# Kernel tuning notes

Measured on AMD Instinct MI355X. Metric: run time of the kernel, lower is better.

The kernel has to match this reference:

```python
import jax, jax.numpy as jnp
import numpy as np

EID, EMB, HID, IN_DIM = 30000, 256, 512, 3
SRC_T, TRG_T, B = 128, 50, 64


def _gru_step(x, h, W_ih, W_hh, b_ih, b_hh):
    # torch GRU gate math. W_ih: [3H, in], W_hh: [3H, H]
    gi = x @ W_ih.T + b_ih
    gh = h @ W_hh.T + b_hh
    i_r, i_z, i_n = jnp.split(gi, 3, axis=1)
    h_r, h_z, h_n = jnp.split(gh, 3, axis=1)
    r = jax.nn.sigmoid(i_r + h_r)
    z = jax.nn.sigmoid(i_z + h_z)
    n = jnp.tanh(i_n + r * h_n)
    return (1.0 - z) * n + z * h


def setup_inputs() -> dict:
    key = jax.random.key(0)
    ks = jax.random.split(key, 24)
    s = 0.05
    inp = {
        "src": jax.random.normal(ks[0], (SRC_T, B, IN_DIM), jnp.float32),
        "src_len": jax.random.randint(ks[1], (B,), SRC_T // 2, SRC_T + 1).astype(jnp.int32),
        "trg_eid": jax.random.randint(ks[2], (TRG_T, B), 0, EID),
        "trg_rate": jax.random.uniform(ks[3], (TRG_T, B), jnp.float32),
        # encoder GRU
        "W_ih_enc": jax.random.normal(ks[4], (3 * HID, IN_DIM), jnp.float32) * s,
        "W_hh_enc": jax.random.normal(ks[5], (3 * HID, HID), jnp.float32) * s,
        "b_ih_enc": jnp.zeros((3 * HID,), jnp.float32),
        "b_hh_enc": jnp.zeros((3 * HID,), jnp.float32),
        # decoder embedding + GRUCell (input = emb + rate_size(1))
        "emb_dec": jax.random.normal(ks[6], (EID, EMB), jnp.float32) * s,
        "W_ih_dec": jax.random.normal(ks[7], (3 * HID, EMB + 1), jnp.float32) * s,
        "W_hh_dec": jax.random.normal(ks[8], (3 * HID, HID), jnp.float32) * s,
        "b_ih_dec": jnp.zeros((3 * HID,), jnp.float32),
        "b_hh_dec": jnp.zeros((3 * HID,), jnp.float32),
        # multi-task block (has its own embedding table)
        "emb_mt": jax.random.normal(ks[9], (EID, EMB), jnp.float32) * s,
        "W_eid": jax.random.normal(ks[10], (EID, HID), jnp.float32) * s,
        "b_eid": jnp.zeros((EID,), jnp.float32),
        "W_r1": jax.random.normal(ks[11], (HID, HID + EMB), jnp.float32) * s,
        "b_r1": jnp.zeros((HID,), jnp.float32),
        "W_r2": jax.random.normal(ks[12], (1, HID), jnp.float32) * s,
        "b_r2": jnp.zeros((1,), jnp.float32),
    }
    return inp


def reference(src, src_len, trg_eid, trg_rate,
              W_ih_enc, W_hh_enc, b_ih_enc, b_hh_enc,
              emb_dec, W_ih_dec, W_hh_dec, b_ih_dec, b_hh_dec,
              emb_mt, W_eid, b_eid, W_r1, b_r1, W_r2, b_r2):
    Bsz = src.shape[1]
    h0 = jnp.zeros((Bsz, HID), src.dtype)

    # --- Encoder: packed GRU == masked scan; final hidden frozen at each seq's length ---
    def enc_step(h, xt_t):
        x_t, t = xt_t
        h_new = _gru_step(x_t, h, W_ih_enc, W_hh_enc, b_ih_enc, b_hh_enc)
        h = jnp.where((t < src_len)[:, None], h_new, h)
        return h, None

    ts = jnp.arange(src.shape[0])
    hidden, _ = jax.lax.scan(enc_step, h0, (src, ts))  # [B, H]

    def dec_step(carry, _):
        h, eid, rate = carry
        x = jnp.concatenate([emb_dec[eid], rate[:, None]], axis=1)  # [B, EMB+1]
        h = _gru_step(x, h, W_ih_dec, W_hh_dec, b_ih_dec, b_hh_dec)
        pre_eid = jax.nn.log_softmax(h @ W_eid.T + b_eid, axis=1)   # [B, EID]
        idx = jnp.argmax(pre_eid, axis=1)
        r1 = jnp.concatenate([emb_mt[idx], h], axis=1) @ W_r1.T + b_r1
        pre_rate = jax.nn.sigmoid((jax.nn.relu(r1) @ W_r2.T + b_r2)[:, 0])  # [B]
        return (h, idx, pre_rate), (pre_eid, pre_rate)

    init = (hidden, trg_eid[0], trg_rate[0])
    _, (eids, rates) = jax.lax.scan(dec_step, init, None, length=TRG_T - 1)

    eid_result = jnp.concatenate([jnp.zeros((1, Bsz, EID), src.dtype), eids], axis=0)
    rate_result = jnp.concatenate([jnp.zeros((1, Bsz), src.dtype), rates], axis=0)
    return eid_result, rate_result
```

## Files before the change

### kernel.cpp

```cpp
#include <hip/hip_runtime.h>
#include <cmath>

#define EIDN  30000
#define EMBN  256
#define HIDN  512
#define INDIM 3
#define SRCT  128
#define TRGT  50
#define BN    64
#define G3H   1536
#define WIH_PAD 260

struct alignas(16) WS {
  float wihd[G3H * WIH_PAD];
  float hb[2][BN][HIDN];
  float rowsum[BN];
  float rate_cur[BN];
  int   eid_cur[BN];
  unsigned long long amax[BN];
};

__device__ __forceinline__ float sigmoidf_(float x) { return 1.f / (1.f + expf(-x)); }

__device__ __forceinline__ unsigned int orderf_(float f) {
  unsigned int b = __float_as_uint(f);
  return b ^ ((b & 0x80000000u) ? 0xFFFFFFFFu : 0x80000000u);
}

__device__ __forceinline__ unsigned long long shfl_down_u64(unsigned long long v, int off, int w) {
  unsigned int lo = (unsigned int)v;
  unsigned int hi = (unsigned int)(v >> 32);
  lo = __shfl_down(lo, off, w);
  hi = __shfl_down(hi, off, w);
  return ((unsigned long long)hi << 32) | (unsigned long long)lo;
}

__device__ __forceinline__ void dot6(const float* __restrict__ x,
                                     const float* const* __restrict__ w,
                                     int n4, float* __restrict__ acc) {
  const float4* x4 = (const float4*)x;
#pragma unroll 4
  for (int k = 0; k < n4; ++k) {
    float4 xv = x4[k];
#pragma unroll
    for (int i = 0; i < 6; ++i) {
      float4 wv = ((const float4*)w[i])[k];
      acc[i] = fmaf(xv.w, wv.w, fmaf(xv.z, wv.z, fmaf(xv.y, wv.y, fmaf(xv.x, wv.x, acc[i]))));
    }
  }
}

__global__ void k_init(const float* __restrict__ Wih_d,
                       const int* __restrict__ trg_eid,
                       const float* __restrict__ trg_rate,
                       float* __restrict__ out, WS* __restrict__ ws) {
  int gid = blockIdx.x * blockDim.x + threadIdx.x;
  int nt = gridDim.x * blockDim.x;
  const int N = G3H * 257;
  for (int i = gid; i < N; i += nt) {
    int r = i / 257, c = i - r * 257;
    ws->wihd[r * WIH_PAD + c] = Wih_d[i];
  }
  float* hb0 = &ws->hb[0][0][0];
  for (int i = gid; i < BN * HIDN; i += nt) hb0[i] = 0.f;
  if (gid < BN) {
    ws->eid_cur[gid]  = trg_eid[gid];
    ws->rate_cur[gid] = trg_rate[gid];
    out[(size_t)TRGT * BN * EIDN + gid] = 0.f;
  }
}

__global__ __launch_bounds__(256) void k_enc_step(
    const float* __restrict__ src, const int* __restrict__ src_len,
    const float* __restrict__ Wih, const float* __restrict__ bih,
    const float* __restrict__ bhh, const float* __restrict__ Whh,
    const float* __restrict__ hin, float* __restrict__ hout, int t) {
  __shared__ float part[BN][4][6];
  int tid = threadIdx.x;
  int b = tid & 63, kq = tid >> 6;
  int j0 = blockIdx.x * 2;

  const float* wrows[6];
#pragma unroll
  for (int idx = 0; idx < 6; ++idx) {
    int u = idx / 3, g = idx - 3 * u;
    wrows[idx] = Whh + (size_t)(g * HIDN + j0 + u) * HIDN + kq * 128;
  }
  float acc[6] = {0.f, 0.f, 0.f, 0.f, 0.f, 0.f};
  dot6(hin + b * HIDN + kq * 128, wrows, 32, acc);
#pragma unroll
  for (int idx = 0; idx < 6; ++idx) part[b][kq][idx] = acc[idx];
  __syncthreads();

  if (kq == 0) {
    int len = src_len[b];
    const float* x = src + ((size_t)t * BN + b) * INDIM;
    float x0 = x[0], x1 = x[1], x2 = x[2];
#pragma unroll
    for (int u = 0; u < 2; ++u) {
      int j = j0 + u;
      float hg[3], ig[3];
#pragma unroll
      for (int g = 0; g < 3; ++g) {
        int idx = u * 3 + g;
        hg[g] = part[b][0][idx] + part[b][1][idx] + part[b][2][idx] + part[b][3][idx]
                + bhh[g * HIDN + j];
        int row = g * HIDN + j;
        ig[g] = bih[row] + x0 * Wih[row * 3] + x1 * Wih[row * 3 + 1] + x2 * Wih[row * 3 + 2];
      }
      float r = sigmoidf_(ig[0] + hg[0]);
      float z = sigmoidf_(ig[1] + hg[1]);
      float n = tanhf(ig[2] + r * hg[2]);
      float ho = hin[b * HIDN + j];
      hout[b * HIDN + j] = (t < len) ? ((1.f - z) * n + z * ho) : ho;
    }
  }
}

__global__ __launch_bounds__(256) void k_dec_gru(
    const float* __restrict__ emb_dec, const float* __restrict__ Whh,
    const float* __restrict__ bih, const float* __restrict__ bhh,
    WS* __restrict__ ws, const float* __restrict__ hin, float* __restrict__ hout) {
  __shared__ float partx[BN][4][6];
  __shared__ float parth[BN][4][6];
  int tid = threadIdx.x;
  if (blockIdx.x == 0 && tid < BN) {
    ws->rowsum[tid] = 0.f;
    ws->amax[tid] = 0ULL;
  }
  int b = tid & 63, kq = tid >> 6;
  int j0 = blockIdx.x * 2;
  int eid = ws->eid_cur[b];
  const float* xe = emb_dec + (size_t)eid * EMBN;
  const float* hrow = hin + b * HIDN;

  float accx[6] = {0.f, 0.f, 0.f, 0.f, 0.f, 0.f};
  float acch[6] = {0.f, 0.f, 0.f, 0.f, 0.f, 0.f};
  const float* w[6];

  if (kq == 0) {
#pragma unroll
    for (int idx = 0; idx < 6; ++idx) {
      int u = idx / 3, g = idx - 3 * u;
      w[idx] = ws->wihd + (size_t)(g * HIDN + j0 + u) * WIH_PAD;
    }
    dot6(xe, w, 48, accx);
  } else if (kq == 1) {
    float rate = ws->rate_cur[b];
#pragma unroll
    for (int idx = 0; idx < 6; ++idx) {
      int u = idx / 3, g = idx - 3 * u;
      const float* wr = ws->wihd + (size_t)(g * HIDN + j0 + u) * WIH_PAD;
      w[idx] = wr + 192;
      accx[idx] = rate * wr[256];
    }
    dot6(xe + 192, w, 16, accx);
#pragma unroll
    for (int idx = 0; idx < 6; ++idx) {
      int u = idx / 3, g = idx - 3 * u;
      w[idx] = Whh + (size_t)(g * HIDN + j0 + u) * HIDN;
    }
    dot6(hrow, w, 32, acch);
  } else {
    int off = (kq == 2) ? 128 : 320;
#pragma unroll
    for (int idx = 0; idx < 6; ++idx) {
      int u = idx / 3, g = idx - 3 * u;
      w[idx] = Whh + (size_t)(g * HIDN + j0 + u) * HIDN + off;
    }
    dot6(hrow + off, w, 48, acch);
  }
#pragma unroll
  for (int idx = 0; idx < 6; ++idx) {
    partx[b][kq][idx] = accx[idx];
    parth[b][kq][idx] = acch[idx];
  }
  __syncthreads();

  if (kq == 0) {
#pragma unroll
    for (int u = 0; u < 2; ++u) {
      int j = j0 + u;
      float ix[3], hh[3];
#pragma unroll
      for (int g = 0; g < 3; ++g) {
        int idx = u * 3 + g;
        ix[g] = partx[b][0][idx] + partx[b][1][idx] + partx[b][2][idx] + partx[b][3][idx]
                + bih[g * HIDN + j];
        hh[g] = parth[b][0][idx] + parth[b][1][idx] + parth[b][2][idx] + parth[b][3][idx]
                + bhh[g * HIDN + j];
      }
      float r = sigmoidf_(ix[0] + hh[0]);
      float z = sigmoidf_(ix[1] + hh[1]);
      float n = tanhf(ix[2] + r * hh[2]);
      hout[b * HIDN + j] = (1.f - z) * n + z * hin[b * HIDN + j];
    }
  }
}

__global__ __launch_bounds__(256) void k_logits(
    const float* __restrict__ Weid, const float* __restrict__ beid,
    const float* __restrict__ h, float* __restrict__ oslice,
    WS* __restrict__ ws) {
  __shared__ float sh[64][68];
  __shared__ float sw[64][68];
  int tid = threadIdx.x;
  int tr = tid >> 4, tc = tid & 15;
  int c0 = blockIdx.x * 64;
  float acc[4][4];
#pragma unroll
  for (int i = 0; i < 4; ++i)
#pragma unroll
    for (int m = 0; m < 4; ++m) acc[i][m] = 0.f;

  for (int kc = 0; kc < 8; ++kc) {
    int k0 = kc * 64;
#pragma unroll
    for (int u = 0; u < 4; ++u) {
      int flat = tid + u * 256;
      int r = flat >> 4, k4 = flat & 15;
      float4 hv = *(const float4*)(h + r * HIDN + k0 + k4 * 4);
      sh[k4 * 4 + 0][r] = hv.x; sh[k4 * 4 + 1][r] = hv.y;
      sh[k4 * 4 + 2][r] = hv.z; sh[k4 * 4 + 3][r] = hv.w;
      int c = c0 + r;
      float4 wv = make_float4(0.f, 0.f, 0.f, 0.f);
      if (c < EIDN) wv = *(const float4*)(Weid + (size_t)c * HIDN + k0 + k4 * 4);
      sw[k4 * 4 + 0][r] = wv.x; sw[k4 * 4 + 1][r] = wv.y;
      sw[k4 * 4 + 2][r] = wv.z; sw[k4 * 4 + 3][r] = wv.w;
    }
    __syncthreads();
#pragma unroll 8
    for (int kk = 0; kk < 64; ++kk) {
      float4 av = *(const float4*)&sh[kk][4 * tr];
      float4 bv = *(const float4*)&sw[kk][4 * tc];
      acc[0][0] = fmaf(av.x, bv.x, acc[0][0]); acc[0][1] = fmaf(av.x, bv.y, acc[0][1]);
      acc[0][2] = fmaf(av.x, bv.z, acc[0][2]); acc[0][3] = fmaf(av.x, bv.w, acc[0][3]);
      acc[1][0] = fmaf(av.y, bv.x, acc[1][0]); acc[1][1] = fmaf(av.y, bv.y, acc[1][1]);
      acc[1][2] = fmaf(av.y, bv.z, acc[1][2]); acc[1][3] = fmaf(av.y, bv.w, acc[1][3]);
      acc[2][0] = fmaf(av.z, bv.x, acc[2][0]); acc[2][1] = fmaf(av.z, bv.y, acc[2][1]);
      acc[2][2] = fmaf(av.z, bv.z, acc[2][2]); acc[2][3] = fmaf(av.z, bv.w, acc[2][3]);
      acc[3][0] = fmaf(av.w, bv.x, acc[3][0]); acc[3][1] = fmaf(av.w, bv.y, acc[3][1]);
      acc[3][2] = fmaf(av.w, bv.z, acc[3][2]); acc[3][3] = fmaf(av.w, bv.w, acc[3][3]);
    }
    __syncthreads();
  }

  int cbase = c0 + 4 * tc;
  float sume[4] = {0.f, 0.f, 0.f, 0.f};
  unsigned long long key[4] = {0ULL, 0ULL, 0ULL, 0ULL};
  if (cbase + 3 < EIDN) {
    float4 bb = *(const float4*)(beid + cbase);
#pragma unroll
    for (int i = 0; i < 4; ++i) {
      float4 L;
      L.x = acc[i][0] + bb.x; L.y = acc[i][1] + bb.y;
      L.z = acc[i][2] + bb.z; L.w = acc[i][3] + bb.w;
      *(float4*)(oslice + (size_t)(4 * tr + i) * EIDN + cbase) = L;
      sume[i] = expf(L.x) + expf(L.y) + expf(L.z) + expf(L.w);
      float lv[4] = {L.x, L.y, L.z, L.w};
#pragma unroll
      for (int cc = 0; cc < 4; ++cc) {
        unsigned long long pk = ((unsigned long long)orderf_(lv[cc]) << 32) |
                                (unsigned long long)(0xFFFFFFFFu - (unsigned)(cbase + cc));
        if (pk > key[i]) key[i] = pk;
      }
    }
  }
#pragma unroll
  for (int off = 8; off > 0; off >>= 1) {
#pragma unroll
    for (int i = 0; i < 4; ++i) {
      sume[i] += __shfl_down(sume[i], off, 16);
      unsigned long long o = shfl_down_u64(key[i], off, 16);
      if (o > key[i]) key[i] = o;
    }
  }
  if (tc == 0) {
#pragma unroll
    for (int i = 0; i < 4; ++i) {
      int r = 4 * tr + i;
      atomicAdd(&ws->rowsum[r], sume[i]);
      atomicMax(&ws->amax[r], key[i]);
    }
  }
}

__global__ __launch_bounds__(256) void k_finalize(
    float* __restrict__ oslice, float* __restrict__ rate_out,
    const float* __restrict__ emb_mt, const float* __restrict__ Wr1,
    const float* __restrict__ br1, const float* __restrict__ Wr2,
    const float* __restrict__ br2, const float* __restrict__ h,
    WS* __restrict__ ws) {
  int tid = threadIdx.x;
  __shared__ float logs[BN];
  if (tid < BN) logs[tid] = logf(ws->rowsum[tid]);
  __syncthreads();
  int gid = blockIdx.x * blockDim.x + tid;
  int nt = gridDim.x * blockDim.x;
  const int nf4 = BN * EIDN / 4;
  const int rowf4 = EIDN / 4;
  float4* o4 = (float4*)oslice;
  for (int f = gid; f < nf4; f += nt) {
    int b = f / rowf4;
    float lb = logs[b];
    float4 v = o4[f];
    v.x -= lb; v.y -= lb; v.z -= lb; v.w -= lb;
    o4[f] = v;
  }
  if (blockIdx.x < BN) {
    int b = blockIdx.x;
    int idx = (int)(0xFFFFFFFFu - (unsigned)(ws->amax[b] & 0xFFFFFFFFull));
    __shared__ float cat[EMBN + HIDN];
    cat[tid]       = emb_mt[(size_t)idx * EMBN + tid];
    cat[EMBN + tid]       = h[b * HIDN + tid];
    cat[EMBN + 256 + tid] = h[b * HIDN + 256 + tid];
    __syncthreads();
    const float4* c4 = (const float4*)cat;
    int j0 = tid * 2;
    const float4* w0 = (const float4*)(Wr1 + (size_t)j0 * (EMBN + HIDN));
    const float4* w1 = (const float4*)(Wr1 + (size_t)(j0 + 1) * (EMBN + HIDN));
    float a0 = br1[j0], a1 = br1[j0 + 1];
#pragma unroll 4
    for (int k = 0; k < (EMBN + HIDN) / 4; ++k) {
      float4 cv = c4[k];
      float4 v0 = w0[k], v1 = w1[k];
      a0 = fmaf(cv.w, v0.w, fmaf(cv.z, v0.z, fmaf(cv.y, v0.y, fmaf(cv.x, v0.x, a0))));
      a1 = fmaf(cv.w, v1.w, fmaf(cv.z, v1.z, fmaf(cv.y, v1.y, fmaf(cv.x, v1.x, a1))));
    }
    float part = fmaxf(a0, 0.f) * Wr2[j0] + fmaxf(a1, 0.f) * Wr2[j0 + 1];
#pragma unroll
    for (int off = 32; off > 0; off >>= 1) part += __shfl_down(part, off, 64);
    __shared__ float wsum[4];
    if ((tid & 63) == 0) wsum[tid >> 6] = part;
    __syncthreads();
    if (tid == 0) {
      float tot = wsum[0] + wsum[1] + wsum[2] + wsum[3] + br2[0];
      float rt = sigmoidf_(tot);
      rate_out[b] = rt;
      ws->rate_cur[b] = rt;
      ws->eid_cur[b] = idx;
    }
  }
}

__global__ void k_zero_t0(float* __restrict__ out) {
  int gid = blockIdx.x * blockDim.x + threadIdx.x;
  int nt = gridDim.x * blockDim.x;
  float4* o4 = (float4*)out;
  for (int f = gid; f < BN * EIDN / 4; f += nt) o4[f] = make_float4(0.f, 0.f, 0.f, 0.f);
}

extern "C" void kernel_launch(void* const* d_in, const int* in_sizes, int n_in,
                              void* d_out, int out_size, void* d_ws, size_t ws_size,
                              hipStream_t stream) {
  const float* src      = (const float*)d_in[0];
  const int*   src_len  = (const int*)d_in[1];
  const int*   trg_eid  = (const int*)d_in[2];
  const float* trg_rate = (const float*)d_in[3];
  const float* Wih_e    = (const float*)d_in[4];
  const float* Whh_e    = (const float*)d_in[5];
  const float* bih_e    = (const float*)d_in[6];
  const float* bhh_e    = (const float*)d_in[7];
  const float* emb_dec  = (const float*)d_in[8];
  const float* Wih_d    = (const float*)d_in[9];
  const float* Whh_d    = (const float*)d_in[10];
  const float* bih_d    = (const float*)d_in[11];
  const float* bhh_d    = (const float*)d_in[12];
  const float* emb_mt   = (const float*)d_in[13];
  const float* Weid     = (const float*)d_in[14];
  const float* beid     = (const float*)d_in[15];
  const float* Wr1      = (const float*)d_in[16];
  const float* br1      = (const float*)d_in[17];
  const float* Wr2      = (const float*)d_in[18];
  const float* br2      = (const float*)d_in[19];
  float* out = (float*)d_out;

  WS* ws = (ws_size >= sizeof(WS)) ? (WS*)d_ws : (WS*)d_out;

  hipLaunchKernelGGL(k_init, dim3(256), dim3(256), 0, stream,
                     Wih_d, trg_eid, trg_rate, out, ws);
  for (int t = 0; t < SRCT; ++t) {
    const float* hin = &ws->hb[t & 1][0][0];
    float* hout = &ws->hb[(t + 1) & 1][0][0];
    hipLaunchKernelGGL(k_enc_step, dim3(256), dim3(256), 0, stream,
                       src, src_len, Wih_e, bih_e, bhh_e, Whh_e, hin, hout, t);
  }
  for (int s = 0; s < TRGT - 1; ++s) {
    const float* hin = &ws->hb[s & 1][0][0];
    float* hout = &ws->hb[(s + 1) & 1][0][0];
    hipLaunchKernelGGL(k_dec_gru, dim3(256), dim3(256), 0, stream,
                       emb_dec, Whh_d, bih_d, bhh_d, ws, hin, hout);
    float* oslice = out + (size_t)(s + 1) * BN * EIDN;
    hipLaunchKernelGGL(k_logits, dim3((EIDN + 63) / 64), dim3(256), 0, stream,
                       Weid, beid, hout, oslice, ws);
    hipLaunchKernelGGL(k_finalize, dim3(512), dim3(256), 0, stream,
                       oslice, out + (size_t)TRGT * BN * EIDN + (size_t)(s + 1) * BN,
                       emb_mt, Wr1, br1, Wr2, br2, hout, ws);
  }
  hipLaunchKernelGGL(k_zero_t0, dim3(480), dim3(256), 0, stream, out);
}
```

Baseline: 9.349 ms.

## Fuse encoder/decoder steps into one persistent kernel with grid-wide barriers

Replaces the roughly 275 per-step kernel launches with a single persistent kernel of 512 workgroups that synchronise through an atomic grid barrier. The logits GEMM keeps its accumulators in registers across the barrier, so the log-softmax normalisation is applied before the single write to output, removing the extra read-modify-write pass over each 64x30000 slice. It also register-prefetches the next K chunk during compute and folds the t0 zeroing into init. The design relies on all 512 workgroups being co-resident (launch bounds of 2 per CU) and on a spin barrier with a timeout guard.

```diff
diff --git a/kernel.cpp b/kernel.cpp
--- a/kernel.cpp
+++ b/kernel.cpp
@@ -10,6 +10,8 @@
 #define BN    64
 #define G3H   1536
 #define WIH_PAD 260
+#define NWG   512
+#define GEMM_WGS 469
 
 struct alignas(16) WS {
   float wihd[G3H * WIH_PAD];
@@ -18,6 +20,14 @@
   float rate_cur[BN];
   int   eid_cur[BN];
   unsigned long long amax[BN];
+  int   bar;
+};
+
+union SMem {
+  float encpart[BN][4][6];
+  struct { float partx[BN][4][6]; float parth[BN][4][6]; } gru;
+  struct { float sh[64][68]; float sw[64][68]; } gemm;
+  struct { float cat[EMBN + HIDN]; float wsum[4]; float logs[BN]; } fin;
 };
 
 __device__ __forceinline__ float sigmoidf_(float x) { return 1.f / (1.f + expf(-x)); }
@@ -33,6 +43,22 @@
   lo = __shfl_down(lo, off, w);
   hi = __shfl_down(hi, off, w);
   return ((unsigned long long)hi << 32) | (unsigned long long)lo;
+}
+
+__device__ __forceinline__ void gsync(int* bar, int& ph) {
+  __syncthreads();
+  if (threadIdx.x == 0) {
+    ++ph;
+    __hip_atomic_fetch_add(bar, 1, __ATOMIC_RELEASE, __HIP_MEMORY_SCOPE_AGENT);
+    const int target = ph * NWG;
+    int guard = 0;
+    while (__hip_atomic_load(bar, __ATOMIC_RELAXED, __HIP_MEMORY_SCOPE_AGENT) < target) {
+      __builtin_amdgcn_s_sleep(2);
+      if (++guard > 20000000) break;
+    }
+    (void)__hip_atomic_load(bar, __ATOMIC_ACQUIRE, __HIP_MEMORY_SCOPE_AGENT);
+  }
+  __syncthreads();
 }
 
 __device__ __forceinline__ void dot6(const float* __restrict__ x,
@@ -50,7 +76,7 @@
   }
 }
 
-__global__ void k_init(const float* __restrict__ Wih_d,
+__global__ __launch_bounds__(256) void k_init(const float* __restrict__ Wih_d,
                        const int* __restrict__ trg_eid,
                        const float* __restrict__ trg_rate,
                        float* __restrict__ out, WS* __restrict__ ws) {
@@ -68,14 +94,16 @@
     ws->rate_cur[gid] = trg_rate[gid];
     out[(size_t)TRGT * BN * EIDN + gid] = 0.f;
   }
-}
-
-__global__ __launch_bounds__(256) void k_enc_step(
+  if (gid == 0) ws->bar = 0;
+  float4* o4 = (float4*)out;
+  for (int f = gid; f < BN * EIDN / 4; f += nt) o4[f] = make_float4(0.f, 0.f, 0.f, 0.f);
+}
+
+__device__ __forceinline__ void enc_step(SMem& sm,
     const float* __restrict__ src, const int* __restrict__ src_len,
     const float* __restrict__ Wih, const float* __restrict__ bih,
     const float* __restrict__ bhh, const float* __restrict__ Whh,
     const float* __restrict__ hin, float* __restrict__ hout, int t) {
-  __shared__ float part[BN][4][6];
   int tid = threadIdx.x;
   int b = tid & 63, kq = tid >> 6;
   int j0 = blockIdx.x * 2;
@@ -89,7 +117,7 @@
   float acc[6] = {0.f, 0.f, 0.f, 0.f, 0.f, 0.f};
   dot6(hin + b * HIDN + kq * 128, wrows, 32, acc);
 #pragma unroll
-  for (int idx = 0; idx < 6; ++idx) part[b][kq][idx] = acc[idx];
+  for (int idx = 0; idx < 6; ++idx) sm.encpart[b][kq][idx] = acc[idx];
   __syncthreads();
 
   if (kq == 0) {
@@ -103,8 +131,8 @@
 #pragma unroll
       for (int g = 0; g < 3; ++g) {
         int idx = u * 3 + g;
-        hg[g] = part[b][0][idx] + part[b][1][idx] + part[b][2][idx] + part[b][3][idx]
-                + bhh[g * HIDN + j];
+        hg[g] = sm.encpart[b][0][idx] + sm.encpart[b][1][idx] + sm.encpart[b][2][idx]
+                + sm.encpart[b][3][idx] + bhh[g * HIDN + j];
         int row = g * HIDN + j;
         ig[g] = bih[row] + x0 * Wih[row * 3] + x1 * Wih[row * 3 + 1] + x2 * Wih[row * 3 + 2];
       }
@@ -117,12 +145,10 @@
   }
 }
 
-__global__ __launch_bounds__(256) void k_dec_gru(
+__device__ __forceinline__ void dec_gru(SMem& sm,
     const float* __restrict__ emb_dec, const float* __restrict__ Whh,
     const float* __restrict__ bih, const float* __restrict__ bhh,
     WS* __restrict__ ws, const float* __restrict__ hin, float* __restrict__ hout) {
-  __shared__ float partx[BN][4][6];
-  __shared__ float parth[BN][4][6];
   int tid = threadIdx.x;
   if (blockIdx.x == 0 && tid < BN) {
     ws->rowsum[tid] = 0.f;
@@ -172,8 +198,8 @@
   }
 #pragma unroll
   for (int idx = 0; idx < 6; ++idx) {
-    partx[b][kq][idx] = accx[idx];
-    parth[b][kq][idx] = acch[idx];
+    sm.gru.partx[b][kq][idx] = accx[idx];
+    sm.gru.parth[b][kq][idx] = acch[idx];
   }
   __syncthreads();
 
@@ -185,10 +211,10 @@
 #pragma unroll
       for (int g = 0; g < 3; ++g) {
         int idx = u * 3 + g;
-        ix[g] = partx[b][0][idx] + partx[b][1][idx] + partx[b][2][idx] + partx[b][3][idx]
-                + bih[g * HIDN + j];
-        hh[g] = parth[b][0][idx] + parth[b][1][idx] + parth[b][2][idx] + parth[b][3][idx]
-                + bhh[g * HIDN + j];
+        ix[g] = sm.gru.partx[b][0][idx] + sm.gru.partx[b][1][idx] + sm.gru.partx[b][2][idx]
+                + sm.gru.partx[b][3][idx] + bih[g * HIDN + j];
+        hh[g] = sm.gru.parth[b][0][idx] + sm.gru.parth[b][1][idx] + sm.gru.parth[b][2][idx]
+                + sm.gru.parth[b][3][idx] + bhh[g * HIDN + j];
       }
       float r = sigmoidf_(ix[0] + hh[0]);
       float z = sigmoidf_(ix[1] + hh[1]);
@@ -198,156 +224,188 @@
   }
 }
 
-__global__ __launch_bounds__(256) void k_logits(
-    const float* __restrict__ Weid, const float* __restrict__ beid,
-    const float* __restrict__ h, float* __restrict__ oslice,
-    WS* __restrict__ ws) {
-  __shared__ float sh[64][68];
-  __shared__ float sw[64][68];
-  int tid = threadIdx.x;
-  int tr = tid >> 4, tc = tid & 15;
-  int c0 = blockIdx.x * 64;
-  float acc[4][4];
-#pragma unroll
-  for (int i = 0; i < 4; ++i)
-#pragma unroll
-    for (int m = 0; m < 4; ++m) acc[i][m] = 0.f;
-
-  for (int kc = 0; kc < 8; ++kc) {
-    int k0 = kc * 64;
-#pragma unroll
-    for (int u = 0; u < 4; ++u) {
-      int flat = tid + u * 256;
-      int r = flat >> 4, k4 = flat & 15;
-      float4 hv = *(const float4*)(h + r * HIDN + k0 + k4 * 4);
-      sh[k4 * 4 + 0][r] = hv.x; sh[k4 * 4 + 1][r] = hv.y;
-      sh[k4 * 4 + 2][r] = hv.z; sh[k4 * 4 + 3][r] = hv.w;
-      int c = c0 + r;
-      float4 wv = make_float4(0.f, 0.f, 0.f, 0.f);
-      if (c < EIDN) wv = *(const float4*)(Weid + (size_t)c * HIDN + k0 + k4 * 4);
-      sw[k4 * 4 + 0][r] = wv.x; sw[k4 * 4 + 1][r] = wv.y;
-      sw[k4 * 4 + 2][r] = wv.z; sw[k4 * 4 + 3][r] = wv.w;
-    }
-    __syncthreads();
-#pragma unroll 8
-    for (int kk = 0; kk < 64; ++kk) {
-      float4 av = *(const float4*)&sh[kk][4 * tr];
-      float4 bv = *(const float4*)&sw[kk][4 * tc];
-      acc[0][0] = fmaf(av.x, bv.x, acc[0][0]); acc[0][1] = fmaf(av.x, bv.y, acc[0][1]);
-      acc[0][2] = fmaf(av.x, bv.z, acc[0][2]); acc[0][3] = fmaf(av.x, bv.w, acc[0][3]);
-      acc[1][0] = fmaf(av.y, bv.x, acc[1][0]); acc[1][1] = fmaf(av.y, bv.y, acc[1][1]);
-      acc[1][2] = fmaf(av.y, bv.z, acc[1][2]); acc[1][3] = fmaf(av.y, bv.w, acc[1][3]);
-      acc[2][0] = fmaf(av.z, bv.x, acc[2][0]); acc[2][1] = fmaf(av.z, bv.y, acc[2][1]);
-      acc[2][2] = fmaf(av.z, bv.z, acc[2][2]); acc[2][3] = fmaf(av.z, bv.w, acc[2][3]);
-      acc[3][0] = fmaf(av.w, bv.x, acc[3][0]); acc[3][1] = fmaf(av.w, bv.y, acc[3][1]);
-      acc[3][2] = fmaf(av.w, bv.z, acc[3][2]); acc[3][3] = fmaf(av.w, bv.w, acc[3][3]);
-    }
-    __syncthreads();
-  }
-
-  int cbase = c0 + 4 * tc;
-  float sume[4] = {0.f, 0.f, 0.f, 0.f};
-  unsigned long long key[4] = {0ULL, 0ULL, 0ULL, 0ULL};
-  if (cbase + 3 < EIDN) {
-    float4 bb = *(const float4*)(beid + cbase);
-#pragma unroll
-    for (int i = 0; i < 4; ++i) {
-      float4 L;
-      L.x = acc[i][0] + bb.x; L.y = acc[i][1] + bb.y;
-      L.z = acc[i][2] + bb.z; L.w = acc[i][3] + bb.w;
-      *(float4*)(oslice + (size_t)(4 * tr + i) * EIDN + cbase) = L;
-      sume[i] = expf(L.x) + expf(L.y) + expf(L.z) + expf(L.w);
-      float lv[4] = {L.x, L.y, L.z, L.w};
-#pragma unroll
-      for (int cc = 0; cc < 4; ++cc) {
-        unsigned long long pk = ((unsigned long long)orderf_(lv[cc]) << 32) |
-                                (unsigned long long)(0xFFFFFFFFu - (unsigned)(cbase + cc));
-        if (pk > key[i]) key[i] = pk;
-      }
-    }
-  }
-#pragma unroll
-  for (int off = 8; off > 0; off >>= 1) {
-#pragma unroll
-    for (int i = 0; i < 4; ++i) {
-      sume[i] += __shfl_down(sume[i], off, 16);
-      unsigned long long o = shfl_down_u64(key[i], off, 16);
-      if (o > key[i]) key[i] = o;
-    }
-  }
-  if (tc == 0) {
-#pragma unroll
-    for (int i = 0; i < 4; ++i) {
-      int r = 4 * tr + i;
-      atomicAdd(&ws->rowsum[r], sume[i]);
-      atomicMax(&ws->amax[r], key[i]);
-    }
-  }
-}
-
-__global__ __launch_bounds__(256) void k_finalize(
-    float* __restrict__ oslice, float* __restrict__ rate_out,
+__device__ __forceinline__ void rate_head(SMem& sm,
     const float* __restrict__ emb_mt, const float* __restrict__ Wr1,
     const float* __restrict__ br1, const float* __restrict__ Wr2,
     const float* __restrict__ br2, const float* __restrict__ h,
-    WS* __restrict__ ws) {
+    WS* __restrict__ ws, float* __restrict__ rate_out) {
   int tid = threadIdx.x;
-  __shared__ float logs[BN];
-  if (tid < BN) logs[tid] = logf(ws->rowsum[tid]);
-  __syncthreads();
-  int gid = blockIdx.x * blockDim.x + tid;
-  int nt = gridDim.x * blockDim.x;
-  const int nf4 = BN * EIDN / 4;
-  const int rowf4 = EIDN / 4;
-  float4* o4 = (float4*)oslice;
-  for (int f = gid; f < nf4; f += nt) {
-    int b = f / rowf4;
-    float lb = logs[b];
-    float4 v = o4[f];
-    v.x -= lb; v.y -= lb; v.z -= lb; v.w -= lb;
-    o4[f] = v;
-  }
-  if (blockIdx.x < BN) {
-    int b = blockIdx.x;
-    int idx = (int)(0xFFFFFFFFu - (unsigned)(ws->amax[b] & 0xFFFFFFFFull));
-    __shared__ float cat[EMBN + HIDN];
-    cat[tid]       = emb_mt[(size_t)idx * EMBN + tid];
-    cat[EMBN + tid]       = h[b * HIDN + tid];
-    cat[EMBN + 256 + tid] = h[b * HIDN + 256 + tid];
-    __syncthreads();
-    const float4* c4 = (const float4*)cat;
-    int j0 = tid * 2;
-    const float4* w0 = (const float4*)(Wr1 + (size_t)j0 * (EMBN + HIDN));
-    const float4* w1 = (const float4*)(Wr1 + (size_t)(j0 + 1) * (EMBN + HIDN));
-    float a0 = br1[j0], a1 = br1[j0 + 1];
+  int b = blockIdx.x;
+  int idx = (int)(0xFFFFFFFFu - (unsigned)(ws->amax[b] & 0xFFFFFFFFull));
+  sm.fin.cat[tid]              = emb_mt[(size_t)idx * EMBN + tid];
+  sm.fin.cat[EMBN + tid]       = h[b * HIDN + tid];
+  sm.fin.cat[EMBN + 256 + tid] = h[b * HIDN + 256 + tid];
+  __syncthreads();
+  const float4* c4 = (const float4*)sm.fin.cat;
+  int j0 = tid * 2;
+  const float4* w0 = (const float4*)(Wr1 + (size_t)j0 * (EMBN + HIDN));
+  const float4* w1 = (const float4*)(Wr1 + (size_t)(j0 + 1) * (EMBN + HIDN));
+  float a0 = br1[j0], a1 = br1[j0 + 1];
 #pragma unroll 4
-    for (int k = 0; k < (EMBN + HIDN) / 4; ++k) {
-      float4 cv = c4[k];
-      float4 v0 = w0[k], v1 = w1[k];
-      a0 = fmaf(cv.w, v0.w, fmaf(cv.z, v0.z, fmaf(cv.y, v0.y, fmaf(cv.x, v0.x, a0))));
-      a1 = fmaf(cv.w, v1.w, fmaf(cv.z, v1.z, fmaf(cv.y, v1.y, fmaf(cv.x, v1.x, a1))));
-    }
-    float part = fmaxf(a0, 0.f) * Wr2[j0] + fmaxf(a1, 0.f) * Wr2[j0 + 1];
-#pragma unroll
-    for (int off = 32; off > 0; off >>= 1) part += __shfl_down(part, off, 64);
-    __shared__ float wsum[4];
-    if ((tid & 63) == 0) wsum[tid >> 6] = part;
-    __syncthreads();
-    if (tid == 0) {
-      float tot = wsum[0] + wsum[1] + wsum[2] + wsum[3] + br2[0];
-      float rt = sigmoidf_(tot);
-      rate_out[b] = rt;
-      ws->rate_cur[b] = rt;
-      ws->eid_cur[b] = idx;
-    }
-  }
-}
-
-__global__ void k_zero_t0(float* __restrict__ out) {
-  int gid = blockIdx.x * blockDim.x + threadIdx.x;
-  int nt = gridDim.x * blockDim.x;
-  float4* o4 = (float4*)out;
-  for (int f = gid; f < BN * EIDN / 4; f += nt) o4[f] = make_float4(0.f, 0.f, 0.f, 0.f);
+  for (int k = 0; k < (EMBN + HIDN) / 4; ++k) {
+    float4 cv = c4[k];
+    float4 v0 = w0[k], v1 = w1[k];
+    a0 = fmaf(cv.w, v0.w, fmaf(cv.z, v0.z, fmaf(cv.y, v0.y, fmaf(cv.x, v0.x, a0))));
+    a1 = fmaf(cv.w, v1.w, fmaf(cv.z, v1.z, fmaf(cv.y, v1.y, fmaf(cv.x, v1.x, a1))));
+  }
+  float part = fmaxf(a0, 0.f) * Wr2[j0] + fmaxf(a1, 0.f) * Wr2[j0 + 1];
+#pragma unroll
+  for (int off = 32; off > 0; off >>= 1) part += __shfl_down(part, off, 64);
+  if ((tid & 63) == 0) sm.fin.wsum[tid >> 6] = part;
+  __syncthreads();
+  if (tid == 0) {
+    float tot = sm.fin.wsum[0] + sm.fin.wsum[1] + sm.fin.wsum[2] + sm.fin.wsum[3] + br2[0];
+    float rt = sigmoidf_(tot);
+    rate_out[b] = rt;
+    ws->rate_cur[b] = rt;
+    ws->eid_cur[b] = idx;
+  }
+}
+
+__global__ __launch_bounds__(256, 2) void k_run(
+    const float* __restrict__ src, const int* __restrict__ src_len,
+    const float* __restrict__ Wih_e, const float* __restrict__ Whh_e,
+    const float* __restrict__ bih_e, const float* __restrict__ bhh_e,
+    const float* __restrict__ emb_dec,
+    const float* __restrict__ Whh_d, const float* __restrict__ bih_d,
+    const float* __restrict__ bhh_d, const float* __restrict__ emb_mt,
+    const float* __restrict__ Weid, const float* __restrict__ beid,
+    const float* __restrict__ Wr1, const float* __restrict__ br1,
+    const float* __restrict__ Wr2, const float* __restrict__ br2,
+    float* __restrict__ out, WS* __restrict__ ws) {
+  __shared__ SMem sm;
+  const int w = blockIdx.x;
+  const int tid = threadIdx.x;
+  const int tr = tid >> 4, tc = tid & 15;
+  int bphase = 0;
+
+  for (int t = 0; t < SRCT; ++t) {
+    const float* hin = &ws->hb[t & 1][0][0];
+    float* hout = &ws->hb[(t + 1) & 1][0][0];
+    if (w < 256) enc_step(sm, src, src_len, Wih_e, bih_e, bhh_e, Whh_e, hin, hout, t);
+    gsync(&ws->bar, bphase);
+  }
+
+  for (int s = 0; s < TRGT - 1; ++s) {
+    const float* hin = &ws->hb[s & 1][0][0];
+    float* hout = &ws->hb[(s + 1) & 1][0][0];
+
+    if (w < 256) dec_gru(sm, emb_dec, Whh_d, bih_d, bhh_d, ws, hin, hout);
+    gsync(&ws->bar, bphase);
+
+    float acc[4][4];
+    bool full = false;
+    const int c0 = w * 64;
+    const int cbase = c0 + 4 * tc;
+    if (w < GEMM_WGS) {
+      full = (cbase + 3 < EIDN);
+      const float* h = hout;
+#pragma unroll
+      for (int i = 0; i < 4; ++i)
+#pragma unroll
+        for (int m = 0; m < 4; ++m) acc[i][m] = 0.f;
+      float4 hv[4], wv[4];
+#pragma unroll
+      for (int u = 0; u < 4; ++u) {
+        int flat = tid + u * 256;
+        int r = flat >> 4, k4 = flat & 15;
+        hv[u] = *(const float4*)(h + r * HIDN + k4 * 4);
+        int c = c0 + r;
+        wv[u] = make_float4(0.f, 0.f, 0.f, 0.f);
+        if (c < EIDN) wv[u] = *(const float4*)(Weid + (size_t)c * HIDN + k4 * 4);
+      }
+      for (int kc = 0; kc < 8; ++kc) {
+#pragma unroll
+        for (int u = 0; u < 4; ++u) {
+          int flat = tid + u * 256;
+          int r = flat >> 4, k4 = flat & 15;
+          sm.gemm.sh[k4 * 4 + 0][r] = hv[u].x; sm.gemm.sh[k4 * 4 + 1][r] = hv[u].y;
+          sm.gemm.sh[k4 * 4 + 2][r] = hv[u].z; sm.gemm.sh[k4 * 4 + 3][r] = hv[u].w;
+          sm.gemm.sw[k4 * 4 + 0][r] = wv[u].x; sm.gemm.sw[k4 * 4 + 1][r] = wv[u].y;
+          sm.gemm.sw[k4 * 4 + 2][r] = wv[u].z; sm.gemm.sw[k4 * 4 + 3][r] = wv[u].w;
+        }
+        __syncthreads();
+        if (kc < 7) {
+          int k0 = (kc + 1) * 64;
+#pragma unroll
+          for (int u = 0; u < 4; ++u) {
+            int flat = tid + u * 256;
+            int r = flat >> 4, k4 = flat & 15;
+            hv[u] = *(const float4*)(h + r * HIDN + k0 + k4 * 4);
+            int c = c0 + r;
+            wv[u] = make_float4(0.f, 0.f, 0.f, 0.f);
+            if (c < EIDN) wv[u] = *(const float4*)(Weid + (size_t)c * HIDN + k0 + k4 * 4);
+          }
+        }
+#pragma unroll 8
+        for (int kk = 0; kk < 64; ++kk) {
+          float4 av = *(const float4*)&sm.gemm.sh[kk][4 * tr];
+          float4 bv = *(const float4*)&sm.gemm.sw[kk][4 * tc];
+          acc[0][0] = fmaf(av.x, bv.x, acc[0][0]); acc[0][1] = fmaf(av.x, bv.y, acc[0][1]);
+          acc[0][2] = fmaf(av.x, bv.z, acc[0][2]); acc[0][3] = fmaf(av.x, bv.w, acc[0][3]);
+          acc[1][0] = fmaf(av.y, bv.x, acc[1][0]); acc[1][1] = fmaf(av.y, bv.y, acc[1][1]);
+          acc[1][2] = fmaf(av.y, bv.z, acc[1][2]); acc[1][3] = fmaf(av.y, bv.w, acc[1][3]);
+          acc[2][0] = fmaf(av.z, bv.x, acc[2][0]); acc[2][1] = fmaf(av.z, bv.y, acc[2][1]);
+          acc[2][2] = fmaf(av.z, bv.z, acc[2][2]); acc[2][3] = fmaf(av.z, bv.w, acc[2][3]);
+          acc[3][0] = fmaf(av.w, bv.x, acc[3][0]); acc[3][1] = fmaf(av.w, bv.y, acc[3][1]);
+          acc[3][2] = fmaf(av.w, bv.z, acc[3][2]); acc[3][3] = fmaf(av.w, bv.w, acc[3][3]);
+        }
+        __syncthreads();
+      }
+      float sume[4] = {0.f, 0.f, 0.f, 0.f};
+      unsigned long long key[4] = {0ULL, 0ULL, 0ULL, 0ULL};
+      if (full) {
+        float4 bb = *(const float4*)(beid + cbase);
+#pragma unroll
+        for (int i = 0; i < 4; ++i) {
+          acc[i][0] += bb.x; acc[i][1] += bb.y; acc[i][2] += bb.z; acc[i][3] += bb.w;
+          sume[i] = expf(acc[i][0]) + expf(acc[i][1]) + expf(acc[i][2]) + expf(acc[i][3]);
+#pragma unroll
+          for (int cc = 0; cc < 4; ++cc) {
+            unsigned long long pk = ((unsigned long long)orderf_(acc[i][cc]) << 32) |
+                                    (unsigned long long)(0xFFFFFFFFu - (unsigned)(cbase + cc));
+            if (pk > key[i]) key[i] = pk;
+          }
+        }
+      }
+#pragma unroll
+      for (int off = 8; off > 0; off >>= 1) {
+#pragma unroll
+        for (int i = 0; i < 4; ++i) {
+          sume[i] += __shfl_down(sume[i], off, 16);
+          unsigned long long o = shfl_down_u64(key[i], off, 16);
+          if (o > key[i]) key[i] = o;
+        }
+      }
+      if (tc == 0) {
+#pragma unroll
+        for (int i = 0; i < 4; ++i) {
+          int r = 4 * tr + i;
+          atomicAdd(&ws->rowsum[r], sume[i]);
+          atomicMax(&ws->amax[r], key[i]);
+        }
+      }
+    }
+    gsync(&ws->bar, bphase);
+
+    float* oslice = out + (size_t)(s + 1) * BN * EIDN;
+    if (w < GEMM_WGS) {
+      if (tid < BN) sm.fin.logs[tid] = logf(ws->rowsum[tid]);
+      __syncthreads();
+      if (full) {
+#pragma unroll
+        for (int i = 0; i < 4; ++i) {
+          float lb = sm.fin.logs[4 * tr + i];
+          float4 L = make_float4(acc[i][0] - lb, acc[i][1] - lb, acc[i][2] - lb, acc[i][3] - lb);
+          *(float4*)(oslice + (size_t)(4 * tr + i) * EIDN + cbase) = L;
+        }
+      }
+    }
+    if (w < BN)
+      rate_head(sm, emb_mt, Wr1, br1, Wr2, br2, hout, ws,
+                out + (size_t)TRGT * BN * EIDN + (size_t)(s + 1) * BN);
+    gsync(&ws->bar, bphase);
+  }
 }
 
 extern "C" void kernel_launch(void* const* d_in, const int* in_sizes, int n_in,
@@ -379,23 +437,8 @@
 
   hipLaunchKernelGGL(k_init, dim3(256), dim3(256), 0, stream,
                      Wih_d, trg_eid, trg_rate, out, ws);
-  for (int t = 0; t < SRCT; ++t) {
-    const float* hin = &ws->hb[t & 1][0][0];
-    float* hout = &ws->hb[(t + 1) & 1][0][0];
-    hipLaunchKernelGGL(k_enc_step, dim3(256), dim3(256), 0, stream,
-                       src, src_len, Wih_e, bih_e, bhh_e, Whh_e, hin, hout, t);
-  }
-  for (int s = 0; s < TRGT - 1; ++s) {
-    const float* hin = &ws->hb[s & 1][0][0];
-    float* hout = &ws->hb[(s + 1) & 1][0][0];
-    hipLaunchKernelGGL(k_dec_gru, dim3(256), dim3(256), 0, stream,
-                       emb_dec, Whh_d, bih_d, bhh_d, ws, hin, hout);
-    float* oslice = out + (size_t)(s + 1) * BN * EIDN;
-    hipLaunchKernelGGL(k_logits, dim3((EIDN + 63) / 64), dim3(256), 0, stream,
-                       Weid, beid, hout, oslice, ws);
-    hipLaunchKernelGGL(k_finalize, dim3(512), dim3(256), 0, stream,
-                       oslice, out + (size_t)TRGT * BN * EIDN + (size_t)(s + 1) * BN,
-                       emb_mt, Wr1, br1, Wr2, br2, hout, ws);
-  }
-  hipLaunchKernelGGL(k_zero_t0, dim3(480), dim3(256), 0, stream, out);
-}
+  hipLaunchKernelGGL(k_run, dim3(NWG), dim3(256), 0, stream,
+                     src, src_len, Wih_e, Whh_e, bih_e, bhh_e,
+                     emb_dec, Whh_d, bih_d, bhh_d, emb_mt,
+                     Weid, beid, Wr1, br1, Wr2, br2, out, ws);
+}
```

New measurement: 18.91 ms. +102.3%, slower.
